# Kernel optimization log

Measured on AMD Instinct MI355X. Metric: run time of the kernel, lower is better.

Reference implementation:

```python
import jax, jax.numpy as jnp
import numpy as np

NUM_HEADS = 16
D_MODEL = 1024


def setup_inputs() -> dict:
    key = jax.random.key(0)
    k1, k2, k3 = jax.random.split(key, 3)
    x = jax.random.normal(k1, (4, 2048, D_MODEL), dtype=jnp.float32)
    # torch.nn.Linear weights are [out_features, in_features]
    w_qkv = jax.random.normal(k2, (3 * D_MODEL, D_MODEL), dtype=jnp.float32) * (1.0 / np.sqrt(D_MODEL))
    w_o = jax.random.normal(k3, (D_MODEL, D_MODEL), dtype=jnp.float32) * (1.0 / np.sqrt(D_MODEL))
    return {"x": x, "w_qkv": w_qkv, "w_o": w_o}


def reference(x, w_qkv, w_o):
    b, n, _ = x.shape
    h = NUM_HEADS
    dh = D_MODEL // h  # head dim
    qkv = jnp.einsum('bnd,ed->bne', x, w_qkv)            # (b, n, 3*d_model)
    # Faithful to: rearrange(qkv, 'b n (h d) -> b h n d', h=h) then chunk(3, dim=-1)
    qkv = qkv.reshape(b, n, h, 3 * dh).transpose(0, 2, 1, 3)  # (b, h, n, 3*dh)
    q, k, v = jnp.split(qkv, 3, axis=-1)                 # each (b, h, n, dh)
    scale = 1.0 / jnp.sqrt(jnp.asarray(dh, dtype=x.dtype))
    scores = jnp.einsum('bhqd,bhkd->bhqk', q, k) * scale  # (b, h, n, n)
    attn = jax.nn.softmax(scores, axis=-1)
    out = jnp.einsum('bhqk,bhkd->bhqd', attn, v)          # (b, h, n, dh)
    out = out.transpose(0, 2, 1, 3).reshape(b, n, h * dh)  # 'b h n d -> b n (h d)'
    return jnp.einsum('bnd,ed->bne', out, w_o)
```

## Files before the change

kernel.cpp:

```cpp
#include <hip/hip_runtime.h>

#define BATCH 4
#define SEQ 2048
#define DM 1024
#define NH 16
#define DH 64
#define M_TOT (BATCH * SEQ)
#define EQKV (3 * DM)
#define QSCALE 0.18033688011112042f

typedef __bf16 bf16x8 __attribute__((ext_vector_type(8)));
typedef unsigned short u16x8 __attribute__((ext_vector_type(8)));
typedef float f32x2 __attribute__((ext_vector_type(2)));
typedef float f32x4 __attribute__((ext_vector_type(4)));
typedef float f32x16 __attribute__((ext_vector_type(16)));

static __device__ __forceinline__ unsigned short f2bf(float f) {
    unsigned int u = __builtin_bit_cast(unsigned int, f);
    u += 0x7fffu + ((u >> 16) & 1u);
    return (unsigned short)(u >> 16);
}

static __device__ __forceinline__ unsigned short f2bf_fast(float f) {
    return (unsigned short)((__builtin_bit_cast(unsigned int, f) + 0x8000u) >> 16);
}

static __device__ __forceinline__ unsigned int cvt_pk_bf16(float lo, float hi) {
    unsigned int r;
    asm("v_cvt_pk_bf16_f32 %0, %1, %2" : "=v"(r) : "v"(lo), "v"(hi));
    return r;
}

static __device__ __forceinline__ f32x2 pk_add(f32x2 a, f32x2 b) {
    f32x2 d;
    asm("v_pk_add_f32 %0, %1, %2" : "=v"(d) : "v"(a), "v"(b));
    return d;
}

static __device__ __forceinline__ float fast_exp2(float x) {
#if __has_builtin(__builtin_amdgcn_exp2f)
    return __builtin_amdgcn_exp2f(x);
#else
    return exp2f(x);
#endif
}

static __device__ __forceinline__ bf16x8 ld_frag(const ushort* p) {
    return *(const bf16x8*)p;
}

static __device__ __forceinline__ bf16x8 mk_frag(unsigned int a, unsigned int b,
                                                 unsigned int c, unsigned int d) {
    union { unsigned int u[4]; bf16x8 v; } t;
    t.u[0] = a; t.u[1] = b; t.u[2] = c; t.u[3] = d;
    return t.v;
}

static __device__ __forceinline__ void gload_lds16(const ushort* g, ushort* l) {
    __builtin_amdgcn_global_load_lds(
        (const __attribute__((address_space(1))) unsigned int*)g,
        (__attribute__((address_space(3))) unsigned int*)l,
        16, 0, 0);
}

__global__ __launch_bounds__(256) void detect_kernel(const ushort* __restrict__ x,
                                                     int* __restrict__ flag) {
    __shared__ int cnt[256];
    const int tid = threadIdx.x;
    int c = 0;
    for (int j = 0; j < 16; ++j) {
        unsigned short w = x[tid * 16 + j];
        int e = (w >> 7) & 0xFF;
        bool sane = (e == 0) || (e >= 0x60 && e <= 0x8F);
        c += sane ? 0 : 1;
    }
    cnt[tid] = c;
    __syncthreads();
    for (int s = 128; s > 0; s >>= 1) {
        if (tid < s) cnt[tid] += cnt[tid + s];
        __syncthreads();
    }
    if (tid == 0) flag[0] = (cnt[0] > 256) ? 1 : 0;
}

__global__ __launch_bounds__(256) void convert_frag_kernel(
    const void* __restrict__ src, ushort* __restrict__ dst, int R,
    const int* __restrict__ flag)
{
    const int t = blockIdx.x * 256 + threadIdx.x;
    if (t >= R * 128) return;
    const int m = t >> 7, kc = t & 127;

    u16x8 v;
    if (flag[0]) {
        const float* s = (const float*)src + (size_t)t * 8;
        #pragma unroll
        for (int j = 0; j < 8; ++j) v[j] = f2bf(s[j]);
    } else {
        v = *((const u16x8*)src + t);
    }
    const size_t o = (((size_t)(m >> 4) * 32 + (kc >> 2)) * 64 + (kc & 3) * 16 + (m & 15)) * 8;
    *(u16x8*)(dst + o) = v;
}

__global__ __launch_bounds__(256) void qkv_gemm_kernel(
    const ushort* __restrict__ XF, const ushort* __restrict__ WF,
    ushort* __restrict__ QF, ushort* __restrict__ KF, ushort* __restrict__ VF)
{
    __shared__ ushort As[2][8 * 512];
    __shared__ ushort Bs[2][8 * 512];

    const int lane = threadIdx.x & 63;
    const int wave = threadIdx.x >> 6;
    const int col  = lane & 15;
    const int quad = lane >> 4;
    const int orig = blockIdx.y * 24 + blockIdx.x;
    const int sid  = (orig & 7) * 192 + (orig >> 3);
    const int bx = sid % 24;
    const int by = sid / 24;
    const int m0 = by * 128 + (wave >> 1) * 64;
    const int e0 = bx * 128 + (wave & 1) * 64;
    const int mt0 = by * 8, et0 = bx * 8;
    const int wa = (wave >> 1) * 4;
    const int wb = (wave & 1) * 4;

    f32x4 acc[4][4];
    #pragma unroll
    for (int i = 0; i < 4; ++i)
        #pragma unroll
        for (int j = 0; j < 4; ++j) acc[i][j] = f32x4{0.f, 0.f, 0.f, 0.f};

#define GSTAGE(kt_, b_) do { \
        _Pragma("unroll") \
        for (int j_ = 0; j_ < 2; ++j_) { \
            const int c_ = wave * 2 + j_; \
            gload_lds16(XF + (size_t)((mt0 + c_) * 32 + (kt_)) * 512 + lane * 8, \
                        &As[b_][c_ * 512]); \
            gload_lds16(WF + (size_t)((et0 + c_) * 32 + (kt_)) * 512 + lane * 8, \
                        &Bs[b_][c_ * 512]); \
        } \
    } while (0)

    GSTAGE(0, 0);
    __syncthreads();

    for (int kt = 0; kt < 32; ++kt) {
        const int cb = kt & 1;
        if (kt + 1 < 32) GSTAGE(kt + 1, cb ^ 1);

        bf16x8 a[4], b[4];
        #pragma unroll
        for (int i = 0; i < 4; ++i) {
            a[i] = ld_frag(&As[cb][(wa + i) * 512] + lane * 8);
            b[i] = ld_frag(&Bs[cb][(wb + i) * 512] + lane * 8);
        }
        #pragma unroll
        for (int i = 0; i < 4; ++i)
            #pragma unroll
            for (int j = 0; j < 4; ++j)
                acc[i][j] = __builtin_amdgcn_mfma_f32_16x16x32_bf16(a[i], b[j], acc[i][j], 0, 0, 0);

        __syncthreads();
    }
#undef GSTAGE

    #pragma unroll
    for (int ej = 0; ej < 4; ++ej) {
        const int e = e0 + ej * 16 + col;
        const int h = e / 192;
        const int c = e - h * 192;
        #pragma unroll
        for (int mi = 0; mi < 4; ++mi) {
            #pragma unroll
            for (int r = 0; r < 4; ++r) {
                const int m = m0 + mi * 16 + quad * 4 + r;
                const int bh = (m >> 11) * NH + h;
                const int n = m & (SEQ - 1);
                const float val = acc[mi][ej][r];
                if (c < 64) {
                    const int d = c;
                    QF[(((size_t)(bh * 64 + (n >> 5)) * 4 + (d >> 4)) * 64
                        + ((d >> 3) & 1) * 32 + (n & 31)) * 8 + (d & 7)] = f2bf_fast(val * QSCALE);
                } else if (c < 128) {
                    const int d = c - 64;
                    KF[(((size_t)(bh * 64 + (n >> 5)) * 4 + (d >> 4)) * 64
                        + ((d >> 3) & 1) * 32 + (n & 31)) * 8 + (d & 7)] = f2bf_fast(val);
                } else {
                    const int d = c - 128;
                    const int r4 = n & 15;
                    const int s4 = (r4 & 3) | (((r4 >> 3) & 1) << 2) | (((r4 >> 2) & 1) << 3);
                    VF[((((size_t)(bh * 32 + (n >> 6)) * 2 + (d >> 5)) * 4 + ((n >> 4) & 3)) * 64
                        + (s4 >> 3) * 32 + (d & 31)) * 8 + (s4 & 7)] = f2bf_fast(val);
                }
            }
        }
    }
}

__global__ __launch_bounds__(256) void attn_kernel(
    const ushort* __restrict__ QF, const ushort* __restrict__ KF,
    const ushort* __restrict__ VF, ushort* __restrict__ AOF)
{
    __shared__ ushort kvs[2][16 * 512];

    const int lane = threadIdx.x & 63;
    const int wave = threadIdx.x >> 6;
    const int half = lane >> 5;
    const int l31  = lane & 31;

    const int i = blockIdx.x;
    const int xcd = i & 7;
    const int s = i >> 3;
    const int qc = s & 15;
    const int bh = ((s >> 4) << 3) | xcd;
    const int q0 = qc * 128 + wave * 32;

    const ushort* qfb = QF + ((size_t)(bh * 64 + (q0 >> 5)) * 4) * 512;
    bf16x8 bq[4];
    #pragma unroll
    for (int d4 = 0; d4 < 4; ++d4) bq[d4] = ld_frag(qfb + d4 * 512 + lane * 8);

    const ushort* kfb = KF + (size_t)bh * 131072;
    const ushort* vfb = VF + (size_t)bh * 131072;

    f32x2 lp0 = {0.f, 0.f}, lp1 = {0.f, 0.f}, lp2 = {0.f, 0.f}, lp3 = {0.f, 0.f};
    f32x16 acc0 = {}, acc1 = {};

#define STAGE(it_, b_) do { \
        const size_t tb_ = (size_t)(it_) * 4096; \
        _Pragma("unroll") \
        for (int j_ = 0; j_ < 4; ++j_) { \
            const int f_ = wave * 4 + j_; \
            const ushort* src_ = (f_ < 8 ? kfb + tb_ + f_ * 512 \
                                         : vfb + tb_ + (f_ - 8) * 512) + lane * 8; \
            gload_lds16(src_, &kvs[b_][f_ * 512]); \
        } \
    } while (0)

#define LACC(v) do { \
        lp0 = pk_add(lp0, __builtin_shufflevector(v, v, 0, 1));   \
        lp1 = pk_add(lp1, __builtin_shufflevector(v, v, 2, 3));   \
        lp2 = pk_add(lp2, __builtin_shufflevector(v, v, 4, 5));   \
        lp3 = pk_add(lp3, __builtin_shufflevector(v, v, 6, 7));   \
        lp0 = pk_add(lp0, __builtin_shufflevector(v, v, 8, 9));   \
        lp1 = pk_add(lp1, __builtin_shufflevector(v, v, 10, 11)); \
        lp2 = pk_add(lp2, __builtin_shufflevector(v, v, 12, 13)); \
        lp3 = pk_add(lp3, __builtin_shufflevector(v, v, 14, 15)); \
    } while (0)

    STAGE(0, 0);
    __syncthreads();

    for (int it = 0; it < 32; ++it) {
        const int cb = it & 1;
        if (it + 1 < 32) STAGE(it + 1, cb ^ 1);

        const ushort* kp = &kvs[cb][0];

        f32x16 st0 = {}, st1 = {};
        #pragma unroll
        for (int d4 = 0; d4 < 4; ++d4) {
            bf16x8 ka0 = ld_frag(kp + d4 * 512 + lane * 8);
            bf16x8 ka1 = ld_frag(kp + (4 + d4) * 512 + lane * 8);
            st0 = __builtin_amdgcn_mfma_f32_32x32x16_bf16(ka0, bq[d4], st0, 0, 0, 0);
            st1 = __builtin_amdgcn_mfma_f32_32x32x16_bf16(ka1, bq[d4], st1, 0, 0, 0);
        }

        bf16x8 va0[4], va1[4];
        #pragma unroll
        for (int f4 = 0; f4 < 4; ++f4) {
            va0[f4] = ld_frag(kp + (8 + f4) * 512 + lane * 8);
            va1[f4] = ld_frag(kp + (12 + f4) * 512 + lane * 8);
        }

        #pragma unroll
        for (int t = 0; t < 16; ++t) st0[t] = fast_exp2(st0[t]);
        #pragma unroll
        for (int t = 0; t < 16; ++t) st1[t] = fast_exp2(st1[t]);
        LACC(st0);
        LACC(st1);

        bf16x8 pf[4];
        pf[0] = mk_frag(cvt_pk_bf16(st0[0],  st0[1]),  cvt_pk_bf16(st0[2],  st0[3]),
                        cvt_pk_bf16(st0[4],  st0[5]),  cvt_pk_bf16(st0[6],  st0[7]));
        pf[1] = mk_frag(cvt_pk_bf16(st0[8],  st0[9]),  cvt_pk_bf16(st0[10], st0[11]),
                        cvt_pk_bf16(st0[12], st0[13]), cvt_pk_bf16(st0[14], st0[15]));
        pf[2] = mk_frag(cvt_pk_bf16(st1[0],  st1[1]),  cvt_pk_bf16(st1[2],  st1[3]),
                        cvt_pk_bf16(st1[4],  st1[5]),  cvt_pk_bf16(st1[6],  st1[7]));
        pf[3] = mk_frag(cvt_pk_bf16(st1[8],  st1[9]),  cvt_pk_bf16(st1[10], st1[11]),
                        cvt_pk_bf16(st1[12], st1[13]), cvt_pk_bf16(st1[14], st1[15]));

        #pragma unroll
        for (int f4 = 0; f4 < 4; ++f4) {
            acc0 = __builtin_amdgcn_mfma_f32_32x32x16_bf16(va0[f4], pf[f4], acc0, 0, 0, 0);
            acc1 = __builtin_amdgcn_mfma_f32_32x32x16_bf16(va1[f4], pf[f4], acc1, 0, 0, 0);
        }

        __syncthreads();
    }
#undef LACC
#undef STAGE

    f32x2 lt = pk_add(pk_add(lp0, lp1), pk_add(lp2, lp3));
    float l_i = lt[0] + lt[1];
    l_i += __shfl_xor(l_i, 32, 64);

    const int b = bh >> 4, h = bh & (NH - 1);
    const float inv = 1.f / l_i;
    const int n_g = b * SEQ + q0 + l31;
    #pragma unroll
    for (int r = 0; r < 16; ++r) {
        const int d = (r & 3) + 8 * (r >> 2) + 4 * half;
        #pragma unroll
        for (int p = 0; p < 2; ++p) {
            const int e = h * 64 + p * 32 + d;
            const float val = (p == 0 ? acc0[r] : acc1[r]) * inv;
            AOF[(((size_t)(n_g >> 4) * 32 + (e >> 5)) * 64
                 + ((e >> 3) & 3) * 16 + (n_g & 15)) * 8 + (e & 7)] = f2bf_fast(val);
        }
    }
}

__global__ __launch_bounds__(256) void out_gemm_kernel(
    const ushort* __restrict__ AOF, const ushort* __restrict__ WOF,
    void* __restrict__ out, const int* __restrict__ flag)
{
    __shared__ ushort As[2][8 * 512];
    __shared__ ushort Bs[2][8 * 512];

    const int lane = threadIdx.x & 63;
    const int wave = threadIdx.x >> 6;
    const int col  = lane & 15;
    const int quad = lane >> 4;
    const int orig = blockIdx.y * 8 + blockIdx.x;
    const int sid  = (orig & 7) * 64 + (orig >> 3);
    const int bx = sid & 7;
    const int by = sid >> 3;
    const int m0 = by * 128 + (wave >> 1) * 64;
    const int e0 = bx * 128 + (wave & 1) * 64;
    const int mt0 = by * 8, et0 = bx * 8;
    const int wa = (wave >> 1) * 4;
    const int wb = (wave & 1) * 4;
    const int f = flag[0];

    f32x4 acc[4][4];
    #pragma unroll
    for (int i = 0; i < 4; ++i)
        #pragma unroll
        for (int j = 0; j < 4; ++j) acc[i][j] = f32x4{0.f, 0.f, 0.f, 0.f};

#define GSTAGE(kt_, b_) do { \
        _Pragma("unroll") \
        for (int j_ = 0; j_ < 2; ++j_) { \
            const int c_ = wave * 2 + j_; \
            gload_lds16(AOF + (size_t)((mt0 + c_) * 32 + (kt_)) * 512 + lane * 8, \
                        &As[b_][c_ * 512]); \
            gload_lds16(WOF + (size_t)((et0 + c_) * 32 + (kt_)) * 512 + lane * 8, \
                        &Bs[b_][c_ * 512]); \
        } \
    } while (0)

    GSTAGE(0, 0);
    __syncthreads();

    for (int kt = 0; kt < 32; ++kt) {
        const int cb = kt & 1;
        if (kt + 1 < 32) GSTAGE(kt + 1, cb ^ 1);

        bf16x8 a[4], b[4];
        #pragma unroll
        for (int i = 0; i < 4; ++i) {
            a[i] = ld_frag(&As[cb][(wa + i) * 512] + lane * 8);
            b[i] = ld_frag(&Bs[cb][(wb + i) * 512] + lane * 8);
        }
        #pragma unroll
        for (int i = 0; i < 4; ++i)
            #pragma unroll
            for (int j = 0; j < 4; ++j)
                acc[i][j] = __builtin_amdgcn_mfma_f32_16x16x32_bf16(a[i], b[j], acc[i][j], 0, 0, 0);

        __syncthreads();
    }
#undef GSTAGE

    if (f == 0) {
        ushort* o = (ushort*)out;
        #pragma unroll
        for (int mi = 0; mi < 4; ++mi)
            #pragma unroll
            for (int ej = 0; ej < 4; ++ej)
                #pragma unroll
                for (int r = 0; r < 4; ++r)
                    o[(size_t)(m0 + mi * 16 + quad * 4 + r) * DM + e0 + ej * 16 + col] = f2bf_fast(acc[mi][ej][r]);
    } else {
        float* o = (float*)out;
        #pragma unroll
        for (int mi = 0; mi < 4; ++mi)
            #pragma unroll
            for (int ej = 0; ej < 4; ++ej)
                #pragma unroll
                for (int r = 0; r < 4; ++r)
                    o[(size_t)(m0 + mi * 16 + quad * 4 + r) * DM + e0 + ej * 16 + col] = acc[mi][ej][r];
    }
}

extern "C" void kernel_launch(void* const* d_in, const int* in_sizes, int n_in,
                              void* d_out, int out_size, void* d_ws, size_t ws_size,
                              hipStream_t stream) {
    const void* x_raw     = d_in[0];
    const void* w_qkv_raw = d_in[1];
    const void* w_o_raw   = d_in[2];

    char* ws = (char*)d_ws;
    int*    flag  = (int*)ws;
    ushort* XF    = (ushort*)(ws + 256);
    ushort* WQKVF = (ushort*)(ws + 256 + (16u << 20));
    ushort* WOF   = (ushort*)(ws + 256 + (22u << 20));
    ushort* QF    = (ushort*)(ws + 256 + (24u << 20));
    ushort* KF    = (ushort*)(ws + 256 + (40u << 20));
    ushort* VF    = (ushort*)(ws + 256 + (56u << 20));
    ushort* AOF   = XF;

    detect_kernel<<<1, 256, 0, stream>>>((const ushort*)x_raw, flag);
    convert_frag_kernel<<<M_TOT / 2, 256, 0, stream>>>(x_raw, XF, M_TOT, flag);
    convert_frag_kernel<<<EQKV / 2, 256, 0, stream>>>(w_qkv_raw, WQKVF, EQKV, flag);
    convert_frag_kernel<<<DM / 2, 256, 0, stream>>>(w_o_raw, WOF, DM, flag);

    qkv_gemm_kernel<<<dim3(EQKV / 128, M_TOT / 128), 256, 0, stream>>>(XF, WQKVF, QF, KF, VF);
    attn_kernel<<<dim3(BATCH * NH * (SEQ / 128)), 256, 0, stream>>>(QF, KF, VF, AOF);
    out_gemm_kernel<<<dim3(DM / 128, M_TOT / 128), 256, 0, stream>>>(AOF, WOF, d_out, flag);
}
```

Before: 297.9 us.

## Use counted vmcnt barriers in GEMM/attention loops and fuse conversion launches

Replaces __syncthreads in the double-buffered loops of the QKV GEMM, attention and output GEMM kernels with explicit barriers. The top barrier waits only until the current stage's loads have landed, leaving the just-issued prefetch in flight, and the end barrier waits only on LDS counters. The three input-conversion launches are merged into one kernel that picks its source by row range and uses vectorized float4 loads. The counted vmcnt(4) relies on each thread issuing exactly four async global-to-LDS loads per stage, so a different stage size would make the wait incorrect.

```diff
diff --git a/kernel.cpp b/kernel.cpp
--- a/kernel.cpp
+++ b/kernel.cpp
@@ -62,6 +62,25 @@
         (__attribute__((address_space(3))) unsigned int*)l,
         16, 0, 0);
 }
+
+#define BAR_TOP_COUNTED() do { \
+        asm volatile("s_waitcnt vmcnt(4)" ::: "memory"); \
+        __builtin_amdgcn_sched_barrier(0); \
+        __builtin_amdgcn_s_barrier(); \
+        __builtin_amdgcn_sched_barrier(0); \
+    } while (0)
+#define BAR_TOP_DRAIN() do { \
+        asm volatile("s_waitcnt vmcnt(0)" ::: "memory"); \
+        __builtin_amdgcn_sched_barrier(0); \
+        __builtin_amdgcn_s_barrier(); \
+        __builtin_amdgcn_sched_barrier(0); \
+    } while (0)
+#define BAR_END() do { \
+        __builtin_amdgcn_sched_barrier(0); \
+        asm volatile("s_waitcnt lgkmcnt(0)" ::: "memory"); \
+        __builtin_amdgcn_s_barrier(); \
+        __builtin_amdgcn_sched_barrier(0); \
+    } while (0)
 
 __global__ __launch_bounds__(256) void detect_kernel(const ushort* __restrict__ x,
                                                      int* __restrict__ flag) {
@@ -83,21 +102,32 @@
     if (tid == 0) flag[0] = (cnt[0] > 256) ? 1 : 0;
 }
 
-__global__ __launch_bounds__(256) void convert_frag_kernel(
-    const void* __restrict__ src, ushort* __restrict__ dst, int R,
+__global__ __launch_bounds__(256) void convert_all_kernel(
+    const void* __restrict__ xs, const void* __restrict__ wqs,
+    const void* __restrict__ wos, ushort* __restrict__ XF,
+    ushort* __restrict__ WQF, ushort* __restrict__ WOF,
     const int* __restrict__ flag)
 {
     const int t = blockIdx.x * 256 + threadIdx.x;
-    if (t >= R * 128) return;
-    const int m = t >> 7, kc = t & 127;
+    const int mg = t >> 7, kc = t & 127;
+
+    const void* src;
+    ushort* dst;
+    int m;
+    if (mg < M_TOT)            { src = xs;  dst = XF;  m = mg; }
+    else if (mg < M_TOT + EQKV){ src = wqs; dst = WQF; m = mg - M_TOT; }
+    else                       { src = wos; dst = WOF; m = mg - (M_TOT + EQKV); }
 
     u16x8 v;
     if (flag[0]) {
-        const float* s = (const float*)src + (size_t)t * 8;
-        #pragma unroll
-        for (int j = 0; j < 8; ++j) v[j] = f2bf(s[j]);
+        const f32x4* s = (const f32x4*)((const float*)src + ((size_t)m * 128 + kc) * 8);
+        const f32x4 lo = s[0], hi = s[1];
+        #pragma unroll
+        for (int j = 0; j < 4; ++j) v[j] = f2bf(lo[j]);
+        #pragma unroll
+        for (int j = 0; j < 4; ++j) v[4 + j] = f2bf(hi[j]);
     } else {
-        v = *((const u16x8*)src + t);
+        v = *((const u16x8*)src + (size_t)m * 128 + kc);
     }
     const size_t o = (((size_t)(m >> 4) * 32 + (kc >> 2)) * 64 + (kc & 3) * 16 + (m & 15)) * 8;
     *(u16x8*)(dst + o) = v;
@@ -142,11 +172,16 @@
     } while (0)
 
     GSTAGE(0, 0);
-    __syncthreads();
+    BAR_TOP_DRAIN();
 
     for (int kt = 0; kt < 32; ++kt) {
         const int cb = kt & 1;
-        if (kt + 1 < 32) GSTAGE(kt + 1, cb ^ 1);
+        if (kt + 1 < 32) {
+            GSTAGE(kt + 1, cb ^ 1);
+            BAR_TOP_COUNTED();
+        } else {
+            BAR_TOP_DRAIN();
+        }
 
         bf16x8 a[4], b[4];
         #pragma unroll
@@ -160,7 +195,7 @@
             for (int j = 0; j < 4; ++j)
                 acc[i][j] = __builtin_amdgcn_mfma_f32_16x16x32_bf16(a[i], b[j], acc[i][j], 0, 0, 0);
 
-        __syncthreads();
+        BAR_END();
     }
 #undef GSTAGE
 
@@ -249,11 +284,16 @@
     } while (0)
 
     STAGE(0, 0);
-    __syncthreads();
+    BAR_TOP_DRAIN();
 
     for (int it = 0; it < 32; ++it) {
         const int cb = it & 1;
-        if (it + 1 < 32) STAGE(it + 1, cb ^ 1);
+        if (it + 1 < 32) {
+            STAGE(it + 1, cb ^ 1);
+            BAR_TOP_COUNTED();
+        } else {
+            BAR_TOP_DRAIN();
+        }
 
         const ushort* kp = &kvs[cb][0];
 
@@ -296,7 +336,7 @@
             acc1 = __builtin_amdgcn_mfma_f32_32x32x16_bf16(va1[f4], pf[f4], acc1, 0, 0, 0);
         }
 
-        __syncthreads();
+        BAR_END();
     }
 #undef LACC
 #undef STAGE
@@ -361,11 +401,16 @@
     } while (0)
 
     GSTAGE(0, 0);
-    __syncthreads();
+    BAR_TOP_DRAIN();
 
     for (int kt = 0; kt < 32; ++kt) {
         const int cb = kt & 1;
-        if (kt + 1 < 32) GSTAGE(kt + 1, cb ^ 1);
+        if (kt + 1 < 32) {
+            GSTAGE(kt + 1, cb ^ 1);
+            BAR_TOP_COUNTED();
+        } else {
+            BAR_TOP_DRAIN();
+        }
 
         bf16x8 a[4], b[4];
         #pragma unroll
@@ -379,7 +424,7 @@
             for (int j = 0; j < 4; ++j)
                 acc[i][j] = __builtin_amdgcn_mfma_f32_16x16x32_bf16(a[i], b[j], acc[i][j], 0, 0, 0);
 
-        __syncthreads();
+        BAR_END();
     }
 #undef GSTAGE
 
@@ -422,9 +467,8 @@
     ushort* AOF   = XF;
 
     detect_kernel<<<1, 256, 0, stream>>>((const ushort*)x_raw, flag);
-    convert_frag_kernel<<<M_TOT / 2, 256, 0, stream>>>(x_raw, XF, M_TOT, flag);
-    convert_frag_kernel<<<EQKV / 2, 256, 0, stream>>>(w_qkv_raw, WQKVF, EQKV, flag);
-    convert_frag_kernel<<<DM / 2, 256, 0, stream>>>(w_o_raw, WOF, DM, flag);
+    convert_all_kernel<<<(M_TOT + EQKV + DM) / 2, 256, 0, stream>>>(
+        x_raw, w_qkv_raw, w_o_raw, XF, WQKVF, WOF, flag);
 
     qkv_gemm_kernel<<<dim3(EQKV / 128, M_TOT / 128), 256, 0, stream>>>(XF, WQKVF, QF, KF, VF);
     attn_kernel<<<dim3(BATCH * NH * (SEQ / 128)), 256, 0, stream>>>(QF, KF, VF, AOF);
```

Result: no change. 295.6 us (-0.8%).
